# Kernel optimization log

Measured on AMD Instinct MI355X. Metric: run time of the kernel, lower is better.

Reference implementation:

```python
import jax, jax.numpy as jnp
import numpy as np

H = 128
K = 4
BN_EPS = 1e-5
BIG = 1e30


def _lin(key, fin, fout):
    k1, k2 = jax.random.split(key)
    bound = 1.0 / np.sqrt(fin)
    W = jax.random.uniform(k1, (fin, fout), jnp.float32, -bound, bound)
    b = jax.random.uniform(k2, (fout,), jnp.float32, -bound, bound)
    return W, b


def setup_inputs() -> dict:
    key = jax.random.key(0)
    ks = jax.random.split(key, 12)
    N = 8192
    x_lc = jax.random.normal(ks[0], (N, 15), jnp.float32)
    batch_lc = jnp.sort(jax.random.randint(ks[1], (N,), 0, 4)).astype(jnp.int64)
    We1, be1 = _lin(ks[2], 15, H)
    We2, be2 = _lin(ks[3], H, H)
    Wc1, bc1 = _lin(ks[4], 2 * H, H)
    Wc2, bc2 = _lin(ks[5], 2 * H, H)
    Wc3, bc3 = _lin(ks[6], 2 * H, H)
    g1 = jnp.ones((H,), jnp.float32); bt1 = jnp.zeros((H,), jnp.float32)
    g2 = jnp.ones((H,), jnp.float32); bt2 = jnp.zeros((H,), jnp.float32)
    g3 = jnp.ones((H,), jnp.float32); bt3 = jnp.zeros((H,), jnp.float32)
    Wo1, bo1 = _lin(ks[7], H, 32)
    Wo2, bo2 = _lin(ks[8], 32, 16)
    Wo3, bo3 = _lin(ks[9], 16, 8)
    return dict(x_lc=x_lc, batch_lc=batch_lc, We1=We1, be1=be1, We2=We2, be2=be2,
                Wc1=Wc1, bc1=bc1, g1=g1, bt1=bt1,
                Wc2=Wc2, bc2=bc2, g2=g2, bt2=bt2,
                Wc3=Wc3, bc3=bc3, g3=g3, bt3=bt3,
                Wo1=Wo1, bo1=bo1, Wo2=Wo2, bo2=bo2, Wo3=Wo3, bo3=bo3)


def knn_idx(x, batch, k):
    # squared euclidean distances within same batch segment, excluding self
    sq = jnp.sum(x * x, axis=-1)                         # [N]
    d2 = sq[:, None] + sq[None, :] - 2.0 * (x @ x.T)     # [N, N]
    same = batch[:, None] == batch[None, :]
    eye = jnp.eye(x.shape[0], dtype=bool)
    d2 = jnp.where(same & ~eye, d2, BIG)
    _, idx = jax.lax.top_k(-d2, k)                       # [N, k] nearest
    return idx


def edge_conv(x, batch, W, b, gamma, beta, use_bn):
    idx = knn_idx(x, batch, K)
    xj = x[idx]                                          # [N, k, H]
    xi = jnp.broadcast_to(x[:, None, :], xj.shape)
    e = jnp.concatenate([xi, xj - xi], axis=-1)          # [N, k, 2H]
    h = jax.nn.elu(e @ W + b)                            # [N, k, H]
    if use_bn:
        m = jnp.mean(h, axis=(0, 1))
        v = jnp.var(h, axis=(0, 1))
        h = (h - m) / jnp.sqrt(v + BN_EPS) * gamma + beta
    return jnp.max(h, axis=1)                            # [N, H]


def reference(x_lc, batch_lc, We1, be1, We2, be2,
              Wc1, bc1, g1, bt1, Wc2, bc2, g2, bt2, Wc3, bc3, g3, bt3,
              Wo1, bo1, Wo2, bo2, Wo3, bo3):
    x = jax.nn.elu(x_lc @ We1 + be1)
    x = jax.nn.elu(x @ We2 + be2)                        # lc_encode
    f1 = edge_conv(x, batch_lc, Wc1, bc1, g1, bt1, True)   # conv1_large
    f2 = f1 + edge_conv(f1, batch_lc, Wc2, bc2, g2, bt2, True)
    f3 = f2 + edge_conv(f2, batch_lc, Wc3, bc3, g3, bt3, True)
    o = jax.nn.elu(f3 @ Wo1 + bo1)                       # dropout = identity (eval)
    o = jax.nn.elu(o @ Wo2 + bo2)
    out = o @ Wo3 + bo3                                  # [N, 8]
    return out
```

## Files before the change

kernel.cpp:

```cpp
#include <hip/hip_runtime.h>
#include <hip/hip_bf16.h>
#include <math.h>

#define N_PTS 8192
#define HD 128
#define BIGF 1e30f
#define IMAX 0x7fffffff

typedef __bf16 bf16x8 __attribute__((ext_vector_type(8)));
typedef float f32x4 __attribute__((ext_vector_type(4)));

__device__ __forceinline__ float elu_f(float x) {
  return x > 0.0f ? x : expm1f(x);
}

__device__ __forceinline__ void gload16(const void* g, const void* l) {
  __builtin_amdgcn_global_load_lds((const __attribute__((address_space(1))) unsigned int*)g,
                                   (__attribute__((address_space(3))) unsigned int*)l,
                                   16, 0, 0);
}

__global__ void segs_kernel(const int* __restrict__ batch32, int* __restrict__ segs) {
  __shared__ int cnt[4];
  __shared__ int is64s;
  const int t = threadIdx.x;
  if (t < 4) cnt[t] = 0;
  if (t == 0) is64s = (batch32[8191] == 0) ? 1 : 0;
  __syncthreads();
  const int is64 = is64s;
  for (int i = t; i < N_PTS; i += blockDim.x) {
    int b = is64 ? batch32[2 * i] : batch32[i];
    atomicAdd(&cnt[b], 1);
  }
  __syncthreads();
  if (t == 0) {
    int s = 0; segs[0] = 0;
    for (int b = 0; b < 4; ++b) { s += cnt[b]; segs[b + 1] = s; }
  }
}

__global__ __launch_bounds__(128) void encode_kernel(
    const float* __restrict__ x_lc,
    const float* __restrict__ We1, const float* __restrict__ be1,
    const float* __restrict__ We2, const float* __restrict__ be2,
    float* __restrict__ out) {
  __shared__ float xr[16 * 15];
  __shared__ float h1[16][128];
  const int r0 = blockIdx.x * 16;
  const int c = threadIdx.x;
  for (int tt = c; tt < 240; tt += 128) xr[tt] = x_lc[r0 * 15 + tt];
  __syncthreads();
  float acc[16];
#pragma unroll
  for (int r = 0; r < 16; ++r) acc[r] = be1[c];
  for (int j = 0; j < 15; ++j) {
    float w = We1[j * 128 + c];
#pragma unroll
    for (int r = 0; r < 16; ++r) acc[r] = fmaf(xr[r * 15 + j], w, acc[r]);
  }
#pragma unroll
  for (int r = 0; r < 16; ++r) h1[r][c] = elu_f(acc[r]);
  __syncthreads();
#pragma unroll
  for (int r = 0; r < 16; ++r) acc[r] = be2[c];
  for (int j0 = 0; j0 < 128; j0 += 4) {
    float w0 = We2[(j0 + 0) * 128 + c];
    float w1 = We2[(j0 + 1) * 128 + c];
    float w2 = We2[(j0 + 2) * 128 + c];
    float w3 = We2[(j0 + 3) * 128 + c];
#pragma unroll
    for (int r = 0; r < 16; ++r) {
      float4 h = *(const float4*)&h1[r][j0];
      acc[r] = fmaf(h.x, w0, acc[r]);
      acc[r] = fmaf(h.y, w1, acc[r]);
      acc[r] = fmaf(h.z, w2, acc[r]);
      acc[r] = fmaf(h.w, w3, acc[r]);
    }
  }
#pragma unroll
  for (int r = 0; r < 16; ++r) out[(r0 + r) * 128 + c] = elu_f(acc[r]);
}

__global__ __launch_bounds__(256) void rownorm_kernel(const float* __restrict__ X,
                                                      float* __restrict__ sq) {
  const int r = blockIdx.x * 256 + threadIdx.x;
  const float4* row = (const float4*)(X + (size_t)r * 128);
  float s = 0.0f;
#pragma unroll
  for (int c = 0; c < 32; ++c) {
    float4 v = row[c];
    s = fmaf(v.x, v.x, s); s = fmaf(v.y, v.y, s);
    s = fmaf(v.z, v.z, s); s = fmaf(v.w, v.w, s);
  }
  sq[r] = s;
}

__global__ __launch_bounds__(256) void tobf16_kernel(const float* __restrict__ X,
                                                     ushort* __restrict__ Xhi,
                                                     ushort* __restrict__ Xlo) {
  const int i = blockIdx.x * 256 + threadIdx.x;
  float4 v = *(const float4*)&X[i * 4];
  float vv[4] = {v.x, v.y, v.z, v.w};
  ushort h[4], l[4];
#pragma unroll
  for (int e = 0; e < 4; ++e) {
    __hip_bfloat16 hb = __float2bfloat16(vv[e]);
    float hf = __bfloat162float(hb);
    __hip_bfloat16 lb = __float2bfloat16(vv[e] - hf);
    h[e] = *(ushort*)&hb; l[e] = *(ushort*)&lb;
  }
  *(ushort4*)&Xhi[i * 4] = make_ushort4(h[0], h[1], h[2], h[3]);
  *(ushort4*)&Xlo[i * 4] = make_ushort4(l[0], l[1], l[2], l[3]);
}

__global__ void prep_pq(const float* __restrict__ W, float* __restrict__ P,
                        float* __restrict__ Q) {
  const int id = blockIdx.x * 256 + threadIdx.x;
  const int k = id >> 7, c = id & 127;
  float top = W[k * 128 + c];
  float bot = W[(k + 128) * 128 + c];
  P[id] = top - bot;
  Q[id] = bot;
}

__device__ __forceinline__ bool lex_less(float da, int ia, float db, int ib) {
  return (da < db) || ((da == db) && (ia < ib));
}
__device__ __forceinline__ void ins4(float d[4], int ix[4], float nd, int ni) {
  if (lex_less(nd, ni, d[3], ix[3])) {
    d[3] = nd; ix[3] = ni;
    if (lex_less(d[3], ix[3], d[2], ix[2])) { float td=d[3];d[3]=d[2];d[2]=td; int ti=ix[3];ix[3]=ix[2];ix[2]=ti; }
    if (lex_less(d[2], ix[2], d[1], ix[1])) { float td=d[2];d[2]=d[1];d[1]=td; int ti=ix[2];ix[2]=ix[1];ix[1]=ti; }
    if (lex_less(d[1], ix[1], d[0], ix[0])) { float td=d[1];d[1]=d[0];d[0]=td; int ti=ix[1];ix[1]=ix[0];ix[0]=ti; }
  }
}

__global__ __launch_bounds__(256, 2) void knn_mfma_kernel(
    const ushort* __restrict__ Xhi, const ushort* __restrict__ Xlo,
    const int* __restrict__ segs, const float* __restrict__ sq,
    float* __restrict__ candD, int* __restrict__ candI) {
  __shared__ __align__(16) char bufA[32768];
  __shared__ __align__(16) char bufB[32768];
  __shared__ float sqj[2][64];

  const int t = threadIdx.x;
  const int w = t >> 6;
  const int lane = t & 63;
  const int ib = blockIdx.x >> 2;
  const int hs = blockIdx.x & 3;
  const int i0 = ib * 32;

  const int rb = w * 4 + (lane >> 4);
  const int c16l = (lane & 15) ^ (rb & 7);
  const int coff = c16l * 8;

#pragma unroll
  for (int c = 0; c < 4; ++c) {
    const ushort* base = (c < 2) ? Xhi : Xlo;
    const ushort* src = base + ((size_t)(i0 + (c & 1) * 16 + rb) * HD + coff);
    gload16(src, bufB + c * 4096 + w * 1024);
  }

  int jloI[2], jhiI[2], iG[2];
#pragma unroll
  for (int a = 0; a < 2; ++a) {
    iG[a] = i0 + a * 16 + (lane & 15);
    int lo = 0, hi = 0;
#pragma unroll
    for (int b = 0; b < 4; ++b) {
      int s = segs[b], e = segs[b + 1];
      if (iG[a] >= s && iG[a] < e) { lo = s; hi = e; }
    }
    jloI[a] = lo; jhiI[a] = hi;
  }
  int jlo_blk = 0, jhi_blk = 0;
  {
    int bf = 0, bl = 0;
#pragma unroll
    for (int b = 0; b < 4; ++b) {
      int s = segs[b], e = segs[b + 1];
      if (i0 >= s && i0 < e) bf = b;
      if (i0 + 31 >= s && i0 + 31 < e) bl = b;
    }
    jlo_blk = segs[bf]; jhi_blk = segs[bl + 1];
  }
  const int len = jhi_blk - jlo_blk;
  const int qlen = (len + 3) >> 2;
  const int jstart = jlo_blk + hs * qlen;
  const int jend = min(jstart + qlen, jhi_blk);
  const int niter = (jend > jstart) ? ((jend - jstart + 63) >> 6) : 0;

  __syncthreads();

  bf16x8 bh[2][4], bl_[2][4];
  {
    const int r15 = lane & 15;
    const int ch = lane >> 4;
#pragma unroll
    for (int ti = 0; ti < 2; ++ti) {
      int row = ti * 16 + r15;
      int sw = row & 7;
#pragma unroll
      for (int kk = 0; kk < 4; ++kk) {
        int off = row * 256 + (((kk * 4 + ch) ^ sw) * 16);
        bh[ti][kk] = *(const bf16x8*)(bufB + off);
        bl_[ti][kk] = *(const bf16x8*)(bufB + 8192 + off);
      }
    }
  }
  asm volatile("s_waitcnt lgkmcnt(0)" ::: "memory");

  if (niter > 0) {
#pragma unroll
    for (int c = 0; c < 8; ++c) {
      const ushort* base = (c < 4) ? Xhi : Xlo;
      int rg = jstart + (c & 3) * 16 + rb;
      if (rg > N_PTS - 1) rg = N_PTS - 1;
      gload16(base + ((size_t)rg * HD + coff), bufA + c * 4096 + w * 1024);
    }
    if (t < 64) sqj[0][t] = sq[min(jstart + t, N_PTS - 1)];
  }

  float bd[2][4]; int bix[2][4];
#pragma unroll
  for (int a = 0; a < 2; ++a)
#pragma unroll
    for (int q = 0; q < 4; ++q) { bd[a][q] = BIGF; bix[a][q] = IMAX; }

  int cur = 0;
  for (int it = 0; it < niter; ++it) {
    const int jt = jstart + (it << 6);
    __syncthreads();
    if (it + 1 < niter) {
      char* dst = cur ? bufA : bufB;
      const int jn = jt + 64;
#pragma unroll
      for (int c = 0; c < 8; ++c) {
        const ushort* base = (c < 4) ? Xhi : Xlo;
        int rg = jn + (c & 3) * 16 + rb;
        if (rg > N_PTS - 1) rg = N_PTS - 1;
        gload16(base + ((size_t)rg * HD + coff), dst + c * 4096 + w * 1024);
      }
      if (t < 64) sqj[cur ^ 1][t] = sq[min(jn + t, N_PTS - 1)];
    }
    const char* bx = cur ? bufB : bufA;

    const int rA = w * 16 + (lane & 15);
    const int swA = rA & 7;
    f32x4 acc0 = {0.f, 0.f, 0.f, 0.f}, acc1 = {0.f, 0.f, 0.f, 0.f};
#pragma unroll
    for (int kk = 0; kk < 4; ++kk) {
      int off = rA * 256 + (((kk * 4 + (lane >> 4)) ^ swA) * 16);
      bf16x8 ahi = *(const bf16x8*)(bx + off);
      bf16x8 alo = *(const bf16x8*)(bx + 16384 + off);
      acc0 = __builtin_amdgcn_mfma_f32_16x16x32_bf16(ahi, bh[0][kk], acc0, 0, 0, 0);
      acc1 = __builtin_amdgcn_mfma_f32_16x16x32_bf16(ahi, bh[1][kk], acc1, 0, 0, 0);
      acc0 = __builtin_amdgcn_mfma_f32_16x16x32_bf16(ahi, bl_[0][kk], acc0, 0, 0, 0);
      acc1 = __builtin_amdgcn_mfma_f32_16x16x32_bf16(ahi, bl_[1][kk], acc1, 0, 0, 0);
      acc0 = __builtin_amdgcn_mfma_f32_16x16x32_bf16(alo, bh[0][kk], acc0, 0, 0, 0);
      acc1 = __builtin_amdgcn_mfma_f32_16x16x32_bf16(alo, bh[1][kk], acc1, 0, 0, 0);
    }
#pragma unroll
    for (int q = 0; q < 4; ++q) {
      const int jl = w * 16 + (lane >> 4) * 4 + q;
      const int jgl = jt + jl;
      const float sj = sqj[cur][jl];
      float key0 = fmaf(-2.0f, acc0[q], sj);
      bool v0 = (jgl < jend) && (jgl >= jloI[0]) && (jgl < jhiI[0]) && (jgl != iG[0]);
      ins4(bd[0], bix[0], v0 ? key0 : BIGF, v0 ? jgl : IMAX);
      float key1 = fmaf(-2.0f, acc1[q], sj);
      bool v1 = (jgl < jend) && (jgl >= jloI[1]) && (jgl < jhiI[1]) && (jgl != iG[1]);
      ins4(bd[1], bix[1], v1 ? key1 : BIGF, v1 ? jgl : IMAX);
    }
    cur ^= 1;
  }

  __syncthreads();
  float (*cd)[68] = (float(*)[68])bufA;
  int (*ci)[68] = (int(*)[68])(bufA + 32 * 68 * 4);
#pragma unroll
  for (int ti = 0; ti < 2; ++ti) {
    int row = ti * 16 + (lane & 15);
    int slot = w * 16 + (lane >> 4) * 4;
#pragma unroll
    for (int q = 0; q < 4; ++q) {
      cd[row][slot + q] = bd[ti][q];
      ci[row][slot + q] = bix[ti][q];
    }
  }
  __syncthreads();
  if (t < 32) {
    float d[4] = {BIGF, BIGF, BIGF, BIGF};
    int ix[4] = {IMAX, IMAX, IMAX, IMAX};
    for (int e = 0; e < 64; ++e) ins4(d, ix, cd[t][e], ci[t][e]);
    const int i = i0 + t;
#pragma unroll
    for (int q = 0; q < 4; ++q) {
      candD[((size_t)hs * N_PTS + i) * 4 + q] = d[q];
      candI[((size_t)hs * N_PTS + i) * 4 + q] = ix[q];
    }
  }
}

__global__ __launch_bounds__(256) void knn_merge(const float* __restrict__ candD,
                                                 const int* __restrict__ candI,
                                                 int* __restrict__ idx_out) {
  const int i = blockIdx.x * 256 + threadIdx.x;
  float d[4] = {BIGF, BIGF, BIGF, BIGF};
  int ix[4] = {IMAX, IMAX, IMAX, IMAX};
#pragma unroll
  for (int h = 0; h < 4; ++h) {
    float4 dd = *(const float4*)&candD[((size_t)h * N_PTS + i) * 4];
    int4 ii = *(const int4*)&candI[((size_t)h * N_PTS + i) * 4];
    ins4(d, ix, dd.x, ii.x); ins4(d, ix, dd.y, ii.y);
    ins4(d, ix, dd.z, ii.z); ins4(d, ix, dd.w, ii.w);
  }
#pragma unroll
  for (int q = 0; q < 4; ++q) {
    int v = ix[q];
    if (v > N_PTS - 1) v = 0;
    idx_out[i * 4 + q] = v;
  }
}

__global__ __launch_bounds__(256) void uv_kernel(
    const float* __restrict__ X, const float* __restrict__ P,
    const float* __restrict__ Q, const float* __restrict__ bias,
    float* __restrict__ U, float* __restrict__ V) {
  __shared__ float xs[16][129];
  const int t = threadIdx.x;
  const int r0 = blockIdx.x * 16;
#pragma unroll
  for (int v = 0; v < 2; ++v) {
    int lin = t + v * 256;
    int r = lin >> 5, c4 = lin & 31;
    float4 val = *(const float4*)&X[(size_t)(r0 + r) * 128 + c4 * 4];
    xs[r][c4 * 4 + 0] = val.x; xs[r][c4 * 4 + 1] = val.y;
    xs[r][c4 * 4 + 2] = val.z; xs[r][c4 * 4 + 3] = val.w;
  }
  __syncthreads();
  const int cg = t & 31, rg = t >> 5;
  const int c0 = cg * 4;
  float4 b4 = *(const float4*)&bias[c0];
  float4 u0 = b4, u1 = b4;
  float4 v0 = make_float4(0, 0, 0, 0), v1 = make_float4(0, 0, 0, 0);
#pragma unroll 8
  for (int k = 0; k < 128; ++k) {
    float4 p = *(const float4*)&P[k * 128 + c0];
    float4 q = *(const float4*)&Q[k * 128 + c0];
    float xa = xs[rg * 2 + 0][k], xb = xs[rg * 2 + 1][k];
    u0.x = fmaf(xa, p.x, u0.x); u0.y = fmaf(xa, p.y, u0.y);
    u0.z = fmaf(xa, p.z, u0.z); u0.w = fmaf(xa, p.w, u0.w);
    u1.x = fmaf(xb, p.x, u1.x); u1.y = fmaf(xb, p.y, u1.y);
    u1.z = fmaf(xb, p.z, u1.z); u1.w = fmaf(xb, p.w, u1.w);
    v0.x = fmaf(xa, q.x, v0.x); v0.y = fmaf(xa, q.y, v0.y);
    v0.z = fmaf(xa, q.z, v0.z); v0.w = fmaf(xa, q.w, v0.w);
    v1.x = fmaf(xb, q.x, v1.x); v1.y = fmaf(xb, q.y, v1.y);
    v1.z = fmaf(xb, q.z, v1.z); v1.w = fmaf(xb, q.w, v1.w);
  }
  const int ra = r0 + rg * 2, rbw = ra + 1;
  *(float4*)&U[(size_t)ra * 128 + c0] = u0;
  *(float4*)&U[(size_t)rbw * 128 + c0] = u1;
  *(float4*)&V[(size_t)ra * 128 + c0] = v0;
  *(float4*)&V[(size_t)rbw * 128 + c0] = v1;
}

__global__ __launch_bounds__(256) void stats_kernel(
    const float* __restrict__ U, const float* __restrict__ V,
    const int* __restrict__ idx, float* __restrict__ part) {
  __shared__ float ps[2][128], ps2[2][128];
  const int t = threadIdx.x;
  const int c = t & 127, half = t >> 7;
  const int r0 = blockIdx.x * 64 + half * 32;
  float s = 0.0f, s2 = 0.0f;
  for (int rr = 0; rr < 32; ++rr) {
    const int i = r0 + rr;
    const float u = U[(size_t)i * 128 + c];
    const int4 jj = *(const int4*)&idx[i * 4];
    float h0 = elu_f(u + V[(size_t)jj.x * 128 + c]);
    float h1 = elu_f(u + V[(size_t)jj.y * 128 + c]);
    float h2 = elu_f(u + V[(size_t)jj.z * 128 + c]);
    float h3 = elu_f(u + V[(size_t)jj.w * 128 + c]);
    s += h0 + h1 + h2 + h3;
    s2 = fmaf(h0, h0, s2); s2 = fmaf(h1, h1, s2);
    s2 = fmaf(h2, h2, s2); s2 = fmaf(h3, h3, s2);
  }
  ps[half][c] = s; ps2[half][c] = s2;
  __syncthreads();
  if (t < 128) {
    part[blockIdx.x * 256 + t] = ps[0][t] + ps[1][t];
    part[blockIdx.x * 256 + 128 + t] = ps2[0][t] + ps2[1][t];
  }
}

__global__ void finalize_kernel(const float* __restrict__ part,
                                const float* __restrict__ g,
                                const float* __restrict__ bt,
                                float* __restrict__ sAB) {
  const int c = threadIdx.x;
  float s = 0.0f, s2 = 0.0f;
  for (int b = 0; b < 128; ++b) {
    s += part[b * 256 + c];
    s2 += part[b * 256 + 128 + c];
  }
  const float inv_n = 1.0f / 32768.0f;
  float mean = s * inv_n;
  float var = s2 * inv_n - mean * mean;
  float inv = 1.0f / sqrtf(var + 1e-5f);
  float sA = g[c] * inv;
  sAB[c] = sA;
  sAB[128 + c] = bt[c] - mean * sA;
}

__global__ __launch_bounds__(256) void pass2_kernel(
    const float* __restrict__ U, const float* __restrict__ V,
    const int* __restrict__ idx, const float* __restrict__ sAB,
    const float* __restrict__ res, float* __restrict__ out) {
  const int t = threadIdx.x;
  const int c = t & 127, half = t >> 7;
  const int r0 = blockIdx.x * 64 + half * 32;
  const float sA = sAB[c], sB = sAB[128 + c];
  for (int rr = 0; rr < 32; ++rr) {
    const int i = r0 + rr;
    const float u = U[(size_t)i * 128 + c];
    const int4 jj = *(const int4*)&idx[i * 4];
    float m = fmaf(elu_f(u + V[(size_t)jj.x * 128 + c]), sA, sB);
    m = fmaxf(m, fmaf(elu_f(u + V[(size_t)jj.y * 128 + c]), sA, sB));
    m = fmaxf(m, fmaf(elu_f(u + V[(size_t)jj.z * 128 + c]), sA, sB));
    m = fmaxf(m, fmaf(elu_f(u + V[(size_t)jj.w * 128 + c]), sA, sB));
    if (res != nullptr) m += res[(size_t)i * 128 + c];
    out[(size_t)i * 128 + c] = m;
  }
}

__global__ __launch_bounds__(256) void mlp_kernel(
    const float* __restrict__ F,
    const float* __restrict__ Wo1, const float* __restrict__ bo1,
    const float* __restrict__ Wo2, const float* __restrict__ bo2,
    const float* __restrict__ Wo3, const float* __restrict__ bo3,
    float* __restrict__ out) {
  __shared__ float xs[8][128];
  __shared__ float o1s[8][33];
  __shared__ float o2s[8][17];
  const int t = threadIdx.x;
  const int r0 = blockIdx.x * 8;
  {
    int r = t >> 5, c4 = t & 31;
    *(float4*)&xs[r][c4 * 4] = *(const float4*)&F[(size_t)(r0 + r) * 128 + c4 * 4];
  }
  __syncthreads();
  const int r = t >> 5, c = t & 31;
  {
    float acc = bo1[c];
    for (int j = 0; j < 128; ++j) acc = fmaf(xs[r][j], Wo1[j * 32 + c], acc);
    o1s[r][c] = elu_f(acc);
  }
  __syncthreads();
  if (c < 16) {
    float acc = bo2[c];
#pragma unroll
    for (int j = 0; j < 32; ++j) acc = fmaf(o1s[r][j], Wo2[j * 16 + c], acc);
    o2s[r][c] = elu_f(acc);
  }
  __syncthreads();
  if (c < 8) {
    float acc = bo3[c];
#pragma unroll
    for (int j = 0; j < 16; ++j) acc = fmaf(o2s[r][j], Wo3[j * 8 + c], acc);
    out[(size_t)(r0 + r) * 8 + c] = acc;
  }
}

extern "C" void kernel_launch(void* const* d_in, const int* in_sizes, int n_in,
                              void* d_out, int out_size, void* d_ws, size_t ws_size,
                              hipStream_t stream) {
  (void)in_sizes; (void)n_in; (void)out_size; (void)ws_size;
  const float* x_lc = (const float*)d_in[0];
  const int* batch = (const int*)d_in[1];
  const float* We1 = (const float*)d_in[2];
  const float* be1 = (const float*)d_in[3];
  const float* We2 = (const float*)d_in[4];
  const float* be2 = (const float*)d_in[5];
  const float* Wc[3] = {(const float*)d_in[6], (const float*)d_in[10], (const float*)d_in[14]};
  const float* bc[3] = {(const float*)d_in[7], (const float*)d_in[11], (const float*)d_in[15]};
  const float* gg[3] = {(const float*)d_in[8], (const float*)d_in[12], (const float*)d_in[16]};
  const float* bt[3] = {(const float*)d_in[9], (const float*)d_in[13], (const float*)d_in[17]};
  const float* Wo1 = (const float*)d_in[18]; const float* bo1 = (const float*)d_in[19];
  const float* Wo2 = (const float*)d_in[20]; const float* bo2 = (const float*)d_in[21];
  const float* Wo3 = (const float*)d_in[22]; const float* bo3 = (const float*)d_in[23];
  float* out = (float*)d_out;

  float* ws = (float*)d_ws;
  float* featA = ws;
  float* featB = featA + N_PTS * HD;
  float* U = featB + N_PTS * HD;
  float* V = U + N_PTS * HD;
  float* sq = V + N_PTS * HD;
  float* Pb = sq + N_PTS;
  float* Qb = Pb + 16384;
  float* part = Qb + 16384;
  float* sAB = part + 128 * 256;
  float* candD = sAB + 256;
  int* candI = (int*)(candD + 4 * N_PTS * 4);
  int* idxb = candI + 4 * N_PTS * 4;
  int* segs = idxb + N_PTS * 4;
  ushort* Xhi = (ushort*)(segs + 8);
  ushort* Xlo = Xhi + N_PTS * HD;

  segs_kernel<<<1, 256, 0, stream>>>(batch, segs);
  encode_kernel<<<512, 128, 0, stream>>>(x_lc, We1, be1, We2, be2, featA);

  float* bufs[2] = {featA, featB};
  int cur = 0;
  for (int cc = 0; cc < 3; ++cc) {
    const float* Xc = bufs[cur];
    float* Onext = bufs[cur ^ 1];
    const float* rs = (cc == 0) ? nullptr : Xc;

    prep_pq<<<64, 256, 0, stream>>>(Wc[cc], Pb, Qb);
    rownorm_kernel<<<32, 256, 0, stream>>>(Xc, sq);
    tobf16_kernel<<<1024, 256, 0, stream>>>(Xc, Xhi, Xlo);
    knn_mfma_kernel<<<1024, 256, 0, stream>>>(Xhi, Xlo, segs, sq, candD, candI);
    knn_merge<<<32, 256, 0, stream>>>(candD, candI, idxb);
    uv_kernel<<<512, 256, 0, stream>>>(Xc, Pb, Qb, bc[cc], U, V);
    stats_kernel<<<128, 256, 0, stream>>>(U, V, idxb, part);
    finalize_kernel<<<1, 128, 0, stream>>>(part, gg[cc], bt[cc], sAB);
    pass2_kernel<<<128, 256, 0, stream>>>(U, V, idxb, sAB, rs, Onext);
    cur ^= 1;
  }

  mlp_kernel<<<1024, 256, 0, stream>>>(bufs[cur], Wo1, bo1, Wo2, bo2, Wo3, bo3, out);
}
```

Baseline: 752.3 us.

## Load KNN tiles directly from global, fuse row norm into bf16 split, batch weight prep

The KNN MFMA kernel drops its LDS double-buffered global_load_lds pipeline and barriers. Each wave now loads its own 16-row j tile and the i-fragments straight from global memory into registers, with the shared buffer kept only for the final candidate merge, which cuts LDS use and should allow more blocks per CU. The row-norm and bf16 hi/lo split kernels are fused into one prep_x kernel that reduces squared norms with a warp shuffle. The three P/Q weight preparations are hoisted into a single launch before the loop. The risk is that direct global loads without LDS staging expose more memory latency and repeat reads of the same X rows across waves.

```diff
diff --git a/kernel.cpp b/kernel.cpp
--- a/kernel.cpp
+++ b/kernel.cpp
@@ -12,12 +12,6 @@
 
 __device__ __forceinline__ float elu_f(float x) {
   return x > 0.0f ? x : expm1f(x);
-}
-
-__device__ __forceinline__ void gload16(const void* g, const void* l) {
-  __builtin_amdgcn_global_load_lds((const __attribute__((address_space(1))) unsigned int*)g,
-                                   (__attribute__((address_space(3))) unsigned int*)l,
-                                   16, 0, 0);
 }
 
 __global__ void segs_kernel(const int* __restrict__ batch32, int* __restrict__ segs) {
@@ -81,25 +75,15 @@
   for (int r = 0; r < 16; ++r) out[(r0 + r) * 128 + c] = elu_f(acc[r]);
 }
 
-__global__ __launch_bounds__(256) void rownorm_kernel(const float* __restrict__ X,
-                                                      float* __restrict__ sq) {
-  const int r = blockIdx.x * 256 + threadIdx.x;
-  const float4* row = (const float4*)(X + (size_t)r * 128);
-  float s = 0.0f;
-#pragma unroll
-  for (int c = 0; c < 32; ++c) {
-    float4 v = row[c];
-    s = fmaf(v.x, v.x, s); s = fmaf(v.y, v.y, s);
-    s = fmaf(v.z, v.z, s); s = fmaf(v.w, v.w, s);
-  }
-  sq[r] = s;
-}
-
-__global__ __launch_bounds__(256) void tobf16_kernel(const float* __restrict__ X,
-                                                     ushort* __restrict__ Xhi,
-                                                     ushort* __restrict__ Xlo) {
-  const int i = blockIdx.x * 256 + threadIdx.x;
-  float4 v = *(const float4*)&X[i * 4];
+__global__ __launch_bounds__(256) void prep_x(const float* __restrict__ X,
+                                              ushort* __restrict__ Xhi,
+                                              ushort* __restrict__ Xlo,
+                                              float* __restrict__ sq) {
+  const int t = threadIdx.x;
+  const int ln = t & 31;
+  const int g = t >> 5;
+  const int r = blockIdx.x * 8 + g;
+  float4 v = *(const float4*)&X[(size_t)r * 128 + ln * 4];
   float vv[4] = {v.x, v.y, v.z, v.w};
   ushort h[4], l[4];
 #pragma unroll
@@ -109,14 +93,22 @@
     __hip_bfloat16 lb = __float2bfloat16(vv[e] - hf);
     h[e] = *(ushort*)&hb; l[e] = *(ushort*)&lb;
   }
-  *(ushort4*)&Xhi[i * 4] = make_ushort4(h[0], h[1], h[2], h[3]);
-  *(ushort4*)&Xlo[i * 4] = make_ushort4(l[0], l[1], l[2], l[3]);
-}
-
-__global__ void prep_pq(const float* __restrict__ W, float* __restrict__ P,
-                        float* __restrict__ Q) {
+  *(ushort4*)&Xhi[(size_t)r * 128 + ln * 4] = make_ushort4(h[0], h[1], h[2], h[3]);
+  *(ushort4*)&Xlo[(size_t)r * 128 + ln * 4] = make_ushort4(l[0], l[1], l[2], l[3]);
+  float s = v.x * v.x;
+  s = fmaf(v.y, v.y, s); s = fmaf(v.z, v.z, s); s = fmaf(v.w, v.w, s);
+#pragma unroll
+  for (int off = 1; off < 32; off <<= 1) s += __shfl_xor(s, off);
+  if (ln == 0) sq[r] = s;
+}
+
+__global__ void prep_pq_all(const float* __restrict__ W0, const float* __restrict__ W1,
+                            const float* __restrict__ W2,
+                            float* __restrict__ P, float* __restrict__ Q) {
   const int id = blockIdx.x * 256 + threadIdx.x;
-  const int k = id >> 7, c = id & 127;
+  const int cc = id >> 14, r = id & 16383;
+  const float* W = (cc == 0) ? W0 : ((cc == 1) ? W1 : W2);
+  const int k = r >> 7, c = r & 127;
   float top = W[k * 128 + c];
   float bot = W[(k + 128) * 128 + c];
   P[id] = top - bot;
@@ -139,9 +131,7 @@
     const ushort* __restrict__ Xhi, const ushort* __restrict__ Xlo,
     const int* __restrict__ segs, const float* __restrict__ sq,
     float* __restrict__ candD, int* __restrict__ candI) {
-  __shared__ __align__(16) char bufA[32768];
-  __shared__ __align__(16) char bufB[32768];
-  __shared__ float sqj[2][64];
+  __shared__ __align__(16) char mbuf[17408];
 
   const int t = threadIdx.x;
   const int w = t >> 6;
@@ -149,22 +139,13 @@
   const int ib = blockIdx.x >> 2;
   const int hs = blockIdx.x & 3;
   const int i0 = ib * 32;
-
-  const int rb = w * 4 + (lane >> 4);
-  const int c16l = (lane & 15) ^ (rb & 7);
-  const int coff = c16l * 8;
-
-#pragma unroll
-  for (int c = 0; c < 4; ++c) {
-    const ushort* base = (c < 2) ? Xhi : Xlo;
-    const ushort* src = base + ((size_t)(i0 + (c & 1) * 16 + rb) * HD + coff);
-    gload16(src, bufB + c * 4096 + w * 1024);
-  }
+  const int r15 = lane & 15;
+  const int ch = lane >> 4;
 
   int jloI[2], jhiI[2], iG[2];
 #pragma unroll
   for (int a = 0; a < 2; ++a) {
-    iG[a] = i0 + a * 16 + (lane & 15);
+    iG[a] = i0 + a * 16 + r15;
     int lo = 0, hi = 0;
 #pragma unroll
     for (int b = 0; b < 4; ++b) {
@@ -188,38 +169,16 @@
   const int qlen = (len + 3) >> 2;
   const int jstart = jlo_blk + hs * qlen;
   const int jend = min(jstart + qlen, jhi_blk);
-  const int niter = (jend > jstart) ? ((jend - jstart + 63) >> 6) : 0;
-
-  __syncthreads();
 
   bf16x8 bh[2][4], bl_[2][4];
-  {
-    const int r15 = lane & 15;
-    const int ch = lane >> 4;
-#pragma unroll
-    for (int ti = 0; ti < 2; ++ti) {
-      int row = ti * 16 + r15;
-      int sw = row & 7;
-#pragma unroll
-      for (int kk = 0; kk < 4; ++kk) {
-        int off = row * 256 + (((kk * 4 + ch) ^ sw) * 16);
-        bh[ti][kk] = *(const bf16x8*)(bufB + off);
-        bl_[ti][kk] = *(const bf16x8*)(bufB + 8192 + off);
-      }
-    }
-  }
-  asm volatile("s_waitcnt lgkmcnt(0)" ::: "memory");
-
-  if (niter > 0) {
-#pragma unroll
-    for (int c = 0; c < 8; ++c) {
-      const ushort* base = (c < 4) ? Xhi : Xlo;
-      int rg = jstart + (c & 3) * 16 + rb;
-      if (rg > N_PTS - 1) rg = N_PTS - 1;
-      gload16(base + ((size_t)rg * HD + coff), bufA + c * 4096 + w * 1024);
-    }
-    if (t < 64) sqj[0][t] = sq[min(jstart + t, N_PTS - 1)];
-  }
+#pragma unroll
+  for (int ti = 0; ti < 2; ++ti)
+#pragma unroll
+    for (int kk = 0; kk < 4; ++kk) {
+      size_t off = (size_t)(i0 + ti * 16 + r15) * HD + (kk * 4 + ch) * 8;
+      bh[ti][kk] = *(const bf16x8*)(Xhi + off);
+      bl_[ti][kk] = *(const bf16x8*)(Xlo + off);
+    }
 
   float bd[2][4]; int bix[2][4];
 #pragma unroll
@@ -227,44 +186,35 @@
 #pragma unroll
     for (int q = 0; q < 4; ++q) { bd[a][q] = BIGF; bix[a][q] = IMAX; }
 
-  int cur = 0;
-  for (int it = 0; it < niter; ++it) {
-    const int jt = jstart + (it << 6);
-    __syncthreads();
-    if (it + 1 < niter) {
-      char* dst = cur ? bufA : bufB;
-      const int jn = jt + 64;
-#pragma unroll
-      for (int c = 0; c < 8; ++c) {
-        const ushort* base = (c < 4) ? Xhi : Xlo;
-        int rg = jn + (c & 3) * 16 + rb;
-        if (rg > N_PTS - 1) rg = N_PTS - 1;
-        gload16(base + ((size_t)rg * HD + coff), dst + c * 4096 + w * 1024);
-      }
-      if (t < 64) sqj[cur ^ 1][t] = sq[min(jn + t, N_PTS - 1)];
-    }
-    const char* bx = cur ? bufB : bufA;
-
-    const int rA = w * 16 + (lane & 15);
-    const int swA = rA & 7;
+#pragma unroll 2
+  for (int jt = jstart + w * 16; jt < jend; jt += 64) {
+    bf16x8 ah[4], al[4];
+    const int jr = min(jt + r15, N_PTS - 1);
+#pragma unroll
+    for (int kk = 0; kk < 4; ++kk) {
+      size_t off = (size_t)jr * HD + (kk * 4 + ch) * 8;
+      ah[kk] = *(const bf16x8*)(Xhi + off);
+      al[kk] = *(const bf16x8*)(Xlo + off);
+    }
+    float sjv[4];
+#pragma unroll
+    for (int q = 0; q < 4; ++q)
+      sjv[q] = sq[min(jt + ch * 4 + q, N_PTS - 1)];
+
     f32x4 acc0 = {0.f, 0.f, 0.f, 0.f}, acc1 = {0.f, 0.f, 0.f, 0.f};
 #pragma unroll
     for (int kk = 0; kk < 4; ++kk) {
-      int off = rA * 256 + (((kk * 4 + (lane >> 4)) ^ swA) * 16);
-      bf16x8 ahi = *(const bf16x8*)(bx + off);
-      bf16x8 alo = *(const bf16x8*)(bx + 16384 + off);
-      acc0 = __builtin_amdgcn_mfma_f32_16x16x32_bf16(ahi, bh[0][kk], acc0, 0, 0, 0);
-      acc1 = __builtin_amdgcn_mfma_f32_16x16x32_bf16(ahi, bh[1][kk], acc1, 0, 0, 0);
-      acc0 = __builtin_amdgcn_mfma_f32_16x16x32_bf16(ahi, bl_[0][kk], acc0, 0, 0, 0);
-      acc1 = __builtin_amdgcn_mfma_f32_16x16x32_bf16(ahi, bl_[1][kk], acc1, 0, 0, 0);
-      acc0 = __builtin_amdgcn_mfma_f32_16x16x32_bf16(alo, bh[0][kk], acc0, 0, 0, 0);
-      acc1 = __builtin_amdgcn_mfma_f32_16x16x32_bf16(alo, bh[1][kk], acc1, 0, 0, 0);
+      acc0 = __builtin_amdgcn_mfma_f32_16x16x32_bf16(ah[kk], bh[0][kk], acc0, 0, 0, 0);
+      acc1 = __builtin_amdgcn_mfma_f32_16x16x32_bf16(ah[kk], bh[1][kk], acc1, 0, 0, 0);
+      acc0 = __builtin_amdgcn_mfma_f32_16x16x32_bf16(ah[kk], bl_[0][kk], acc0, 0, 0, 0);
+      acc1 = __builtin_amdgcn_mfma_f32_16x16x32_bf16(ah[kk], bl_[1][kk], acc1, 0, 0, 0);
+      acc0 = __builtin_amdgcn_mfma_f32_16x16x32_bf16(al[kk], bh[0][kk], acc0, 0, 0, 0);
+      acc1 = __builtin_amdgcn_mfma_f32_16x16x32_bf16(al[kk], bh[1][kk], acc1, 0, 0, 0);
     }
 #pragma unroll
     for (int q = 0; q < 4; ++q) {
-      const int jl = w * 16 + (lane >> 4) * 4 + q;
-      const int jgl = jt + jl;
-      const float sj = sqj[cur][jl];
+      const int jgl = jt + ch * 4 + q;
+      const float sj = sjv[q];
       float key0 = fmaf(-2.0f, acc0[q], sj);
       bool v0 = (jgl < jend) && (jgl >= jloI[0]) && (jgl < jhiI[0]) && (jgl != iG[0]);
       ins4(bd[0], bix[0], v0 ? key0 : BIGF, v0 ? jgl : IMAX);
@@ -272,16 +222,15 @@
       bool v1 = (jgl < jend) && (jgl >= jloI[1]) && (jgl < jhiI[1]) && (jgl != iG[1]);
       ins4(bd[1], bix[1], v1 ? key1 : BIGF, v1 ? jgl : IMAX);
     }
-    cur ^= 1;
-  }
-
-  __syncthreads();
-  float (*cd)[68] = (float(*)[68])bufA;
-  int (*ci)[68] = (int(*)[68])(bufA + 32 * 68 * 4);
+  }
+
+  __syncthreads();
+  float (*cd)[68] = (float(*)[68])mbuf;
+  int (*ci)[68] = (int(*)[68])(mbuf + 32 * 68 * 4);
 #pragma unroll
   for (int ti = 0; ti < 2; ++ti) {
-    int row = ti * 16 + (lane & 15);
-    int slot = w * 16 + (lane >> 4) * 4;
+    int row = ti * 16 + r15;
+    int slot = w * 16 + ch * 4;
 #pragma unroll
     for (int q = 0; q < 4; ++q) {
       cd[row][slot + q] = bd[ti][q];
@@ -356,7 +305,7 @@
     v0.x = fmaf(xa, q.x, v0.x); v0.y = fmaf(xa, q.y, v0.y);
     v0.z = fmaf(xa, q.z, v0.z); v0.w = fmaf(xa, q.w, v0.w);
     v1.x = fmaf(xb, q.x, v1.x); v1.y = fmaf(xb, q.y, v1.y);
-    v1.z = fmaf(xb, q.z, v1.z); v1.w = fmaf(xb, q.w, v1.w);
+    v1.w = fmaf(xb, q.w, v1.w); v1.z = fmaf(xb, q.z, v1.z);
   }
   const int ra = r0 + rg * 2, rbw = ra + 1;
   *(float4*)&U[(size_t)ra * 128 + c0] = u0;
@@ -497,8 +446,8 @@
   float* V = U + N_PTS * HD;
   float* sq = V + N_PTS * HD;
   float* Pb = sq + N_PTS;
-  float* Qb = Pb + 16384;
-  float* part = Qb + 16384;
+  float* Qb = Pb + 3 * 16384;
+  float* part = Qb + 3 * 16384;
   float* sAB = part + 128 * 256;
   float* candD = sAB + 256;
   int* candI = (int*)(candD + 4 * N_PTS * 4);
@@ -509,6 +458,7 @@
 
   segs_kernel<<<1, 256, 0, stream>>>(batch, segs);
   encode_kernel<<<512, 128, 0, stream>>>(x_lc, We1, be1, We2, be2, featA);
+  prep_pq_all<<<192, 256, 0, stream>>>(Wc[0], Wc[1], Wc[2], Pb, Qb);
 
   float* bufs[2] = {featA, featB};
   int cur = 0;
@@ -517,12 +467,10 @@
     float* Onext = bufs[cur ^ 1];
     const float* rs = (cc == 0) ? nullptr : Xc;
 
-    prep_pq<<<64, 256, 0, stream>>>(Wc[cc], Pb, Qb);
-    rownorm_kernel<<<32, 256, 0, stream>>>(Xc, sq);
-    tobf16_kernel<<<1024, 256, 0, stream>>>(Xc, Xhi, Xlo);
+    prep_x<<<1024, 256, 0, stream>>>(Xc, Xhi, Xlo, sq);
     knn_mfma_kernel<<<1024, 256, 0, stream>>>(Xhi, Xlo, segs, sq, candD, candI);
     knn_merge<<<32, 256, 0, stream>>>(candD, candI, idxb);
-    uv_kernel<<<512, 256, 0, stream>>>(Xc, Pb, Qb, bc[cc], U, V);
+    uv_kernel<<<512, 256, 0, stream>>>(Xc, Pb + cc * 16384, Qb + cc * 16384, bc[cc], U, V);
     stats_kernel<<<128, 256, 0, stream>>>(U, V, idxb, part);
     finalize_kernel<<<1, 128, 0, stream>>>(part, gg[cc], bt[cc], sAB);
     pass2_kernel<<<128, 256, 0, stream>>>(U, V, idxb, sAB, rs, Onext);
```

Result: faster. 697.8 us (-7.2%).
